# Optimization experiments

Measured on AMD Instinct MI355X. Metric: run time of the kernel, lower is better.

The kernel has to match this reference:

```python
import jax, jax.numpy as jnp
import numpy as np

# Object condensation loss config (matches init_kwargs / HGCalML defaults)
Q_MIN = 0.5
S_B = 1.0
POT_SCALE = 1.0
REP_SCALE = 1.0
BETA_SCALE = 1.0
E_WEIGHT = 1.0
HUBER_DELTA = 2.0
E_DEN_OFFSET = 1.0
K_MAX = 192          # object-id slots per event; id 0 = noise
EPS = 1e-6

B, N = 4, 50000


def setup_inputs() -> dict:
    key = jax.random.key(0)
    k1, k2, k3, k4, k5 = jax.random.split(key, 5)
    return {
        "beta": jax.random.uniform(k1, (B, N, 1), dtype=jnp.float32),
        "ccoords": jax.random.normal(k2, (B, N, 2), dtype=jnp.float32),
        "pred_energy": jax.random.uniform(k3, (B, N, 1), dtype=jnp.float32),
        "true_energy": jax.random.uniform(k4, (B, N, 1), dtype=jnp.float32),
        "truth_idx": jax.random.randint(k5, (B, N), 0, K_MAX, dtype=jnp.int32),
    }


def _per_event(beta, ccoords, pred_e, true_e, tidx):
    # beta: [N,1], ccoords: [N,2], tidx: [N] int (0 = noise)
    beta = jnp.clip(beta[:, 0], 1e-4, 1.0 - 1e-4)            # [N]
    q = jnp.arctanh(beta) ** 2 + Q_MIN                        # charge  [N]

    ids = jnp.arange(K_MAX)
    M = (tidx[:, None] == ids[None, :]) & (ids[None, :] > 0)  # [N,K] membership
    Mf = M.astype(q.dtype)
    obj_valid = jnp.any(M, axis=0)                            # [K]
    vf = obj_valid.astype(q.dtype)

    # condensation point alpha_k = argmax_q over members of object k
    qM = jnp.where(M, q[:, None], -1.0)                       # [N,K]
    idx_alpha = jnp.argmax(qM, axis=0)                        # [K]
    x_alpha = ccoords[idx_alpha]                              # [K,2]
    q_alpha = q[idx_alpha]                                    # [K]
    beta_alpha = beta[idx_alpha]                              # [K]

    # pairwise hit<->condensation-point distances
    d2 = jnp.sum((ccoords[:, None, :] - x_alpha[None, :, :]) ** 2, axis=-1)  # [N,K]

    # attractive potential (members), repulsive hinge (non-members of valid objects)
    att = jnp.sum(d2 * q_alpha[None, :] * Mf, axis=-1)                       # [N]
    dist = jnp.sqrt(d2 + EPS)
    rep = jnp.sum(jnp.maximum(0.0, 1.0 - dist) * q_alpha[None, :]
                  * (1.0 - Mf) * vf[None, :], axis=-1)                       # [N]
    L_V = jnp.mean(q * (POT_SCALE * att + REP_SCALE * rep))

    n_obj = jnp.sum(vf) + EPS
    L_beta = BETA_SCALE * jnp.sum((1.0 - beta_alpha) * vf) / n_obj

    noise = (tidx == 0).astype(q.dtype)
    L_noise = S_B * jnp.sum(beta * noise) / (jnp.sum(noise) + EPS)

    # energy payload loss: relative error, Huber, beta-weighted per object
    ediff = (pred_e[:, 0] - true_e[:, 0]) / (true_e[:, 0] + E_DEN_OFFSET)
    ad = jnp.abs(ediff)
    eh = jnp.where(ad <= HUBER_DELTA, 0.5 * ad ** 2,
                   HUBER_DELTA * (ad - 0.5 * HUBER_DELTA))                   # [N]
    pw = Mf * beta[:, None]                                                  # [N,K]
    per_obj_e = jnp.sum(pw * eh[:, None], axis=0) / (jnp.sum(pw, axis=0) + EPS)
    L_E = E_WEIGHT * jnp.sum(per_obj_e * vf) / n_obj

    return L_V + L_beta + L_noise + L_E


def reference(beta, ccoords, pred_energy, true_energy, truth_idx):
    per_ev = jax.vmap(_per_event)(beta, ccoords, pred_energy, true_energy, truth_idx)
    return jnp.mean(per_ev)
```

## Files before the change

kernel.cpp:

```cpp
#include <hip/hip_runtime.h>
#include <math.h>

#define KM 192
#define EPSF 1e-6f
#define QMIN 0.5f

__device__ __forceinline__ float clipb(float b) {
    return fminf(fmaxf(b, 1e-4f), 1.0f - 1e-4f);
}

__global__ void k_zero(unsigned int* p, int n) {
    int i = blockIdx.x * blockDim.x + threadIdx.x;
    if (i < n) p[i] = 0u;
}

__global__ void k_argmax(const float* __restrict__ beta, const int* __restrict__ tidx,
                         unsigned long long* __restrict__ packs, int N) {
    const int e = blockIdx.y;
    __shared__ unsigned long long smax[KM];
    for (int k = threadIdx.x; k < KM; k += blockDim.x) smax[k] = 0ull;
    __syncthreads();

    const float* b = beta + (size_t)e * N;
    const int*   t = tidx + (size_t)e * N;
    const int stride = gridDim.x * blockDim.x;
    for (int i = blockIdx.x * blockDim.x + threadIdx.x; i < N; i += stride) {
        int k = t[i];
        if (k > 0) {
            float bc = clipb(b[i]);
            float a  = atanhf(bc);
            float q  = a * a + QMIN;
            unsigned long long pack =
                ((unsigned long long)__float_as_uint(q) << 32) |
                (unsigned long long)(unsigned)(N - 1 - i);
            atomicMax(&smax[k], pack);
        }
    }
    __syncthreads();
    for (int k = threadIdx.x; k < KM; k += blockDim.x)
        if (smax[k]) atomicMax(&packs[e * KM + k], smax[k]);
}

__global__ void k_gather(const float* __restrict__ beta, const float* __restrict__ cc,
                         const unsigned long long* __restrict__ packs,
                         float* __restrict__ xa0, float* __restrict__ xa1,
                         float* __restrict__ qv,  float* __restrict__ vf,
                         float* __restrict__ scal, int N) {
    const int e = blockIdx.x;
    const int k = threadIdx.x;
    float lb = 0.f, nv = 0.f;
    if (k < KM) {
        unsigned long long p = packs[e * KM + k];
        float x0 = 0.f, x1 = 0.f, q = 0.f, v = 0.f;
        if (p) {
            int idx = N - 1 - (int)(unsigned)(p & 0xffffffffull);
            q  = __uint_as_float((unsigned)(p >> 32));
            x0 = cc[((size_t)e * N + idx) * 2 + 0];
            x1 = cc[((size_t)e * N + idx) * 2 + 1];
            float bc = clipb(beta[(size_t)e * N + idx]);
            lb = 1.0f - bc;
            v = 1.f; nv = 1.f;
        }
        xa0[e * KM + k] = x0;
        xa1[e * KM + k] = x1;
        qv [e * KM + k] = q * v;
        vf [e * KM + k] = v;
    }
    __shared__ float r1[256], r2[256];
    r1[threadIdx.x] = lb; r2[threadIdx.x] = nv;
    __syncthreads();
    for (int s = 128; s > 0; s >>= 1) {
        if (threadIdx.x < s) { r1[threadIdx.x] += r1[threadIdx.x + s];
                               r2[threadIdx.x] += r2[threadIdx.x + s]; }
        __syncthreads();
    }
    if (threadIdx.x == 0) { scal[e * 8 + 1] = r1[0];
                            scal[e * 8 + 2] = r2[0]; }
}

__global__ void k_main(const float* __restrict__ beta, const float* __restrict__ cc,
                       const float* __restrict__ pe,   const float* __restrict__ te,
                       const int* __restrict__ tidx,
                       const float* __restrict__ xa0, const float* __restrict__ xa1,
                       const float* __restrict__ qv,
                       float* __restrict__ enum_, float* __restrict__ eden,
                       float* __restrict__ scal, int N) {
    const int e = blockIdx.y;
    __shared__ float s0[KM], s1[KM], sq[KM];
    __shared__ float sn[KM], sd[KM];
    for (int k = threadIdx.x; k < KM; k += blockDim.x) {
        s0[k] = xa0[e * KM + k];
        s1[k] = xa1[e * KM + k];
        sq[k] = qv [e * KM + k];
        sn[k] = 0.f; sd[k] = 0.f;
    }
    __syncthreads();

    float lv = 0.f, bn = 0.f, cn = 0.f;
    const size_t base = (size_t)e * N;
    const int stride = gridDim.x * blockDim.x;
    for (int i = blockIdx.x * blockDim.x + threadIdx.x; i < N; i += stride) {
        float bc = clipb(beta[base + i]);
        float a  = atanhf(bc);
        float q  = a * a + QMIN;
        float cx = cc[(base + i) * 2 + 0];
        float cy = cc[(base + i) * 2 + 1];
        int   t  = tidx[base + i];

        float rep = 0.f;
        #pragma unroll 8
        for (int k = 0; k < KM; ++k) {
            float dx = cx - s0[k], dy = cy - s1[k];
            float d2 = dx * dx + dy * dy;
            float w  = 1.0f - sqrtf(d2 + EPSF);
            rep += fmaxf(w, 0.f) * sq[k];
        }

        float att = 0.f;
        if (t > 0) {
            float dx = cx - s0[t], dy = cy - s1[t];
            float d2 = dx * dx + dy * dy;
            att = d2 * sq[t];
            rep -= fmaxf(1.0f - sqrtf(d2 + EPSF), 0.f) * sq[t];

            float edv = (pe[base + i] - te[base + i]) / (te[base + i] + 1.0f);
            float ad  = fabsf(edv);
            float eh  = (ad <= 2.0f) ? 0.5f * ad * ad : 2.0f * (ad - 1.0f);
            atomicAdd(&sn[t], bc * eh);
            atomicAdd(&sd[t], bc);
        } else {
            bn += bc; cn += 1.f;
        }
        lv += q * (att + rep);
    }
    __syncthreads();

    for (int k = threadIdx.x; k < KM; k += blockDim.x) {
        if (sn[k] != 0.f) atomicAdd(&enum_[e * KM + k], sn[k]);
        if (sd[k] != 0.f) atomicAdd(&eden[e * KM + k], sd[k]);
    }

    __shared__ float ra[256], rb[256], rc[256];
    ra[threadIdx.x] = lv; rb[threadIdx.x] = bn; rc[threadIdx.x] = cn;
    __syncthreads();
    for (int s = 128; s > 0; s >>= 1) {
        if (threadIdx.x < s) { ra[threadIdx.x] += ra[threadIdx.x + s];
                               rb[threadIdx.x] += rb[threadIdx.x + s];
                               rc[threadIdx.x] += rc[threadIdx.x + s]; }
        __syncthreads();
    }
    if (threadIdx.x == 0) {
        atomicAdd(&scal[e * 8 + 0], ra[0]);
        atomicAdd(&scal[e * 8 + 3], rb[0]);
        atomicAdd(&scal[e * 8 + 4], rc[0]);
    }
}

__global__ void k_fin(const float* __restrict__ enum_, const float* __restrict__ eden,
                      const float* __restrict__ vf,    const float* __restrict__ scal,
                      float* __restrict__ out, int B, int N) {
    __shared__ float r[256];
    float tot = 0.f;
    for (int e = 0; e < B; ++e) {
        float le = 0.f;
        for (int k = threadIdx.x; k < KM; k += blockDim.x)
            le += vf[e * KM + k] * enum_[e * KM + k] / (eden[e * KM + k] + EPSF);
        r[threadIdx.x] = le;
        __syncthreads();
        for (int s = 128; s > 0; s >>= 1) {
            if (threadIdx.x < s) r[threadIdx.x] += r[threadIdx.x + s];
            __syncthreads();
        }
        if (threadIdx.x == 0) {
            float nobj = scal[e * 8 + 2] + EPSF;
            float LV = scal[e * 8 + 0] / (float)N;
            float LB = scal[e * 8 + 1] / nobj;
            float LN = scal[e * 8 + 3] / (scal[e * 8 + 4] + EPSF);
            float LE = r[0] / nobj;
            tot += LV + LB + LN + LE;
        }
        __syncthreads();
    }
    if (threadIdx.x == 0) out[0] = tot / (float)B;
}

extern "C" void kernel_launch(void* const* d_in, const int* in_sizes, int n_in,
                              void* d_out, int out_size, void* d_ws, size_t ws_size,
                              hipStream_t stream) {
    const int B = 4;
    const int N = in_sizes[0] / B;

    const float* beta = (const float*)d_in[0];
    const float* cc   = (const float*)d_in[1];
    const float* pe   = (const float*)d_in[2];
    const float* te   = (const float*)d_in[3];
    const int*   tidx = (const int*)  d_in[4];
    float* out = (float*)d_out;

    char* ws = (char*)d_ws;
    unsigned long long* packs = (unsigned long long*)ws;
    float* xa0  = (float*)(ws + (size_t)B * KM * 8);
    float* xa1  = xa0  + B * KM;
    float* qv   = xa1  + B * KM;
    float* vf   = qv   + B * KM;
    float* enm  = vf   + B * KM;
    float* eden = enm  + B * KM;
    float* scal = eden + B * KM;
    const int totalWords = (B * KM * 8) / 4 + B * KM * 6 + B * 8;

    k_zero<<<dim3((totalWords + 255) / 256), dim3(256), 0, stream>>>((unsigned int*)ws, totalWords);
    k_argmax<<<dim3(64, B), dim3(256), 0, stream>>>(beta, tidx, packs, N);
    k_gather<<<dim3(B), dim3(256), 0, stream>>>(beta, cc, packs, xa0, xa1, qv, vf, scal, N);
    k_main<<<dim3(128, B), dim3(256), 0, stream>>>(beta, cc, pe, te, tidx, xa0, xa1, qv, enm, eden, scal, N);
    k_fin<<<dim3(1), dim3(256), 0, stream>>>(enm, eden, vf, scal, out, B, N);
}
```

Before: 118.7 us.

## Fuse gather and finalize into main kernel, one hit per thread

Removes the gather and finalize kernels: the main kernel now decodes condensation points straight from the argmax packs into a float4 shared table, and the last block (found with an atomic counter) computes the final loss. Both argmax and main switch to one hit per thread with many more blocks; main uses 128-thread blocks with wave shuffle reductions and four partial accumulators in the 192-object loop. Zeroing becomes a hipMemsetAsync. This cuts launch count and raises occupancy, at the cost of more per-block shared-memory setup and more global atomics.

```diff
diff --git a/kernel.cpp b/kernel.cpp
--- a/kernel.cpp
+++ b/kernel.cpp
@@ -4,14 +4,10 @@
 #define KM 192
 #define EPSF 1e-6f
 #define QMIN 0.5f
+#define BLK_MAIN 128
 
 __device__ __forceinline__ float clipb(float b) {
     return fminf(fmaxf(b, 1e-4f), 1.0f - 1e-4f);
-}
-
-__global__ void k_zero(unsigned int* p, int n) {
-    int i = blockIdx.x * blockDim.x + threadIdx.x;
-    if (i < n) p[i] = 0u;
 }
 
 __global__ void k_argmax(const float* __restrict__ beta, const int* __restrict__ tidx,
@@ -20,14 +16,11 @@
     __shared__ unsigned long long smax[KM];
     for (int k = threadIdx.x; k < KM; k += blockDim.x) smax[k] = 0ull;
     __syncthreads();
-
-    const float* b = beta + (size_t)e * N;
-    const int*   t = tidx + (size_t)e * N;
-    const int stride = gridDim.x * blockDim.x;
-    for (int i = blockIdx.x * blockDim.x + threadIdx.x; i < N; i += stride) {
-        int k = t[i];
+    const int i = blockIdx.x * blockDim.x + threadIdx.x;
+    if (i < N) {
+        int k = tidx[(size_t)e * N + i];
         if (k > 0) {
-            float bc = clipb(b[i]);
+            float bc = clipb(beta[(size_t)e * N + i]);
             float a  = atanhf(bc);
             float q  = a * a + QMIN;
             unsigned long long pack =
@@ -41,65 +34,38 @@
         if (smax[k]) atomicMax(&packs[e * KM + k], smax[k]);
 }
 
-__global__ void k_gather(const float* __restrict__ beta, const float* __restrict__ cc,
-                         const unsigned long long* __restrict__ packs,
-                         float* __restrict__ xa0, float* __restrict__ xa1,
-                         float* __restrict__ qv,  float* __restrict__ vf,
-                         float* __restrict__ scal, int N) {
-    const int e = blockIdx.x;
-    const int k = threadIdx.x;
-    float lb = 0.f, nv = 0.f;
-    if (k < KM) {
+__global__ void __launch_bounds__(BLK_MAIN)
+k_main(const float* __restrict__ beta, const float* __restrict__ cc,
+       const float* __restrict__ pe,   const float* __restrict__ te,
+       const int* __restrict__ tidx,
+       const unsigned long long* __restrict__ packs,
+       float* __restrict__ enm, float* __restrict__ eden,
+       float* __restrict__ scal, unsigned int* __restrict__ cnt,
+       float* __restrict__ out, int N, int B) {
+    const int e = blockIdx.y;
+    __shared__ float4 sa[KM];
+    __shared__ float  sn[KM], sd[KM];
+    __shared__ float  swred[6];
+    __shared__ int    lastFlag;
+
+    for (int k = threadIdx.x; k < KM; k += BLK_MAIN) {
         unsigned long long p = packs[e * KM + k];
-        float x0 = 0.f, x1 = 0.f, q = 0.f, v = 0.f;
+        float x0 = 0.f, x1 = 0.f, qv = 0.f;
         if (p) {
             int idx = N - 1 - (int)(unsigned)(p & 0xffffffffull);
-            q  = __uint_as_float((unsigned)(p >> 32));
             x0 = cc[((size_t)e * N + idx) * 2 + 0];
             x1 = cc[((size_t)e * N + idx) * 2 + 1];
-            float bc = clipb(beta[(size_t)e * N + idx]);
-            lb = 1.0f - bc;
-            v = 1.f; nv = 1.f;
-        }
-        xa0[e * KM + k] = x0;
-        xa1[e * KM + k] = x1;
-        qv [e * KM + k] = q * v;
-        vf [e * KM + k] = v;
-    }
-    __shared__ float r1[256], r2[256];
-    r1[threadIdx.x] = lb; r2[threadIdx.x] = nv;
-    __syncthreads();
-    for (int s = 128; s > 0; s >>= 1) {
-        if (threadIdx.x < s) { r1[threadIdx.x] += r1[threadIdx.x + s];
-                               r2[threadIdx.x] += r2[threadIdx.x + s]; }
-        __syncthreads();
-    }
-    if (threadIdx.x == 0) { scal[e * 8 + 1] = r1[0];
-                            scal[e * 8 + 2] = r2[0]; }
-}
-
-__global__ void k_main(const float* __restrict__ beta, const float* __restrict__ cc,
-                       const float* __restrict__ pe,   const float* __restrict__ te,
-                       const int* __restrict__ tidx,
-                       const float* __restrict__ xa0, const float* __restrict__ xa1,
-                       const float* __restrict__ qv,
-                       float* __restrict__ enum_, float* __restrict__ eden,
-                       float* __restrict__ scal, int N) {
-    const int e = blockIdx.y;
-    __shared__ float s0[KM], s1[KM], sq[KM];
-    __shared__ float sn[KM], sd[KM];
-    for (int k = threadIdx.x; k < KM; k += blockDim.x) {
-        s0[k] = xa0[e * KM + k];
-        s1[k] = xa1[e * KM + k];
-        sq[k] = qv [e * KM + k];
+            qv = __uint_as_float((unsigned)(p >> 32));
+        }
+        sa[k] = make_float4(x0, x1, qv, 0.f);
         sn[k] = 0.f; sd[k] = 0.f;
     }
     __syncthreads();
 
+    const size_t base = (size_t)e * N;
+    const int i = blockIdx.x * BLK_MAIN + threadIdx.x;
     float lv = 0.f, bn = 0.f, cn = 0.f;
-    const size_t base = (size_t)e * N;
-    const int stride = gridDim.x * blockDim.x;
-    for (int i = blockIdx.x * blockDim.x + threadIdx.x; i < N; i += stride) {
+    if (i < N) {
         float bc = clipb(beta[base + i]);
         float a  = atanhf(bc);
         float q  = a * a + QMIN;
@@ -107,76 +73,105 @@
         float cy = cc[(base + i) * 2 + 1];
         int   t  = tidx[base + i];
 
-        float rep = 0.f;
-        #pragma unroll 8
+        float racc[4] = {0.f, 0.f, 0.f, 0.f};
+        #pragma unroll 16
         for (int k = 0; k < KM; ++k) {
-            float dx = cx - s0[k], dy = cy - s1[k];
-            float d2 = dx * dx + dy * dy;
-            float w  = 1.0f - sqrtf(d2 + EPSF);
-            rep += fmaxf(w, 0.f) * sq[k];
-        }
+            float4 av = sa[k];
+            float dx = cx - av.x, dy = cy - av.y;
+            float d2 = fmaf(dx, dx, fmaf(dy, dy, EPSF));
+            racc[k & 3] += fmaxf(1.f - sqrtf(d2), 0.f) * av.z;
+        }
+        float rep = (racc[0] + racc[1]) + (racc[2] + racc[3]);
 
         float att = 0.f;
         if (t > 0) {
-            float dx = cx - s0[t], dy = cy - s1[t];
-            float d2 = dx * dx + dy * dy;
-            att = d2 * sq[t];
-            rep -= fmaxf(1.0f - sqrtf(d2 + EPSF), 0.f) * sq[t];
-
-            float edv = (pe[base + i] - te[base + i]) / (te[base + i] + 1.0f);
+            float4 ao = sa[t];
+            float dx = cx - ao.x, dy = cy - ao.y;
+            float d2e = fmaf(dx, dx, fmaf(dy, dy, EPSF));
+            rep -= fmaxf(1.f - sqrtf(d2e), 0.f) * ao.z;
+            att  = fmaf(dx, dx, dy * dy) * ao.z;
+
+            float tev = te[base + i];
+            float edv = (pe[base + i] - tev) / (tev + 1.f);
             float ad  = fabsf(edv);
-            float eh  = (ad <= 2.0f) ? 0.5f * ad * ad : 2.0f * (ad - 1.0f);
+            float eh  = (ad <= 2.f) ? 0.5f * ad * ad : 2.f * (ad - 1.f);
             atomicAdd(&sn[t], bc * eh);
             atomicAdd(&sd[t], bc);
         } else {
-            bn += bc; cn += 1.f;
-        }
-        lv += q * (att + rep);
-    }
-    __syncthreads();
-
-    for (int k = threadIdx.x; k < KM; k += blockDim.x) {
-        if (sn[k] != 0.f) atomicAdd(&enum_[e * KM + k], sn[k]);
-        if (sd[k] != 0.f) atomicAdd(&eden[e * KM + k], sd[k]);
-    }
-
-    __shared__ float ra[256], rb[256], rc[256];
-    ra[threadIdx.x] = lv; rb[threadIdx.x] = bn; rc[threadIdx.x] = cn;
-    __syncthreads();
-    for (int s = 128; s > 0; s >>= 1) {
-        if (threadIdx.x < s) { ra[threadIdx.x] += ra[threadIdx.x + s];
-                               rb[threadIdx.x] += rb[threadIdx.x + s];
-                               rc[threadIdx.x] += rc[threadIdx.x + s]; }
+            bn = bc; cn = 1.f;
+        }
+        lv = q * (att + rep);
+    }
+    __syncthreads();
+
+    for (int k = threadIdx.x; k < KM; k += BLK_MAIN) {
+        float vd = sd[k];
+        if (vd != 0.f) {
+            atomicAdd(&enm [e * KM + k], sn[k]);
+            atomicAdd(&eden[e * KM + k], vd);
+        }
+    }
+
+    for (int off = 32; off > 0; off >>= 1) {
+        lv += __shfl_down(lv, off);
+        bn += __shfl_down(bn, off);
+        cn += __shfl_down(cn, off);
+    }
+    const int wid = threadIdx.x >> 6;
+    if ((threadIdx.x & 63) == 0) {
+        swred[wid] = lv; swred[2 + wid] = bn; swred[4 + wid] = cn;
+    }
+    __syncthreads();
+    if (threadIdx.x == 0) {
+        atomicAdd(&scal[e * 8 + 0], swred[0] + swred[1]);
+        atomicAdd(&scal[e * 8 + 3], swred[2] + swred[3]);
+        atomicAdd(&scal[e * 8 + 4], swred[4] + swred[5]);
+    }
+
+    if (threadIdx.x == 0) {
+        __threadfence();
+        unsigned int total = gridDim.x * gridDim.y;
+        unsigned int old = atomicAdd(cnt, 1u);
+        lastFlag = (old == total - 1u);
+    }
+    __syncthreads();
+    if (!lastFlag) return;
+
+    __threadfence();
+    volatile float* venm  = enm;
+    volatile float* veden = eden;
+    volatile float* vscal = scal;
+
+    float tot = 0.f;
+    for (int ev = 0; ev < B; ++ev) {
+        float lb = 0.f, nv = 0.f, le = 0.f;
+        for (int k = threadIdx.x; k < KM; k += BLK_MAIN) {
+            unsigned long long p = packs[ev * KM + k];
+            if (p) {
+                int idx = N - 1 - (int)(unsigned)(p & 0xffffffffull);
+                lb += 1.f - clipb(beta[(size_t)ev * N + idx]);
+                nv += 1.f;
+                le += venm[ev * KM + k] / (veden[ev * KM + k] + EPSF);
+            }
+        }
+        for (int off = 32; off > 0; off >>= 1) {
+            lb += __shfl_down(lb, off);
+            nv += __shfl_down(nv, off);
+            le += __shfl_down(le, off);
+        }
         __syncthreads();
-    }
-    if (threadIdx.x == 0) {
-        atomicAdd(&scal[e * 8 + 0], ra[0]);
-        atomicAdd(&scal[e * 8 + 3], rb[0]);
-        atomicAdd(&scal[e * 8 + 4], rc[0]);
-    }
-}
-
-__global__ void k_fin(const float* __restrict__ enum_, const float* __restrict__ eden,
-                      const float* __restrict__ vf,    const float* __restrict__ scal,
-                      float* __restrict__ out, int B, int N) {
-    __shared__ float r[256];
-    float tot = 0.f;
-    for (int e = 0; e < B; ++e) {
-        float le = 0.f;
-        for (int k = threadIdx.x; k < KM; k += blockDim.x)
-            le += vf[e * KM + k] * enum_[e * KM + k] / (eden[e * KM + k] + EPSF);
-        r[threadIdx.x] = le;
+        if ((threadIdx.x & 63) == 0) {
+            sn[threadIdx.x >> 6] = lb; sn[2 + (threadIdx.x >> 6)] = nv;
+            sn[4 + (threadIdx.x >> 6)] = le;
+        }
         __syncthreads();
-        for (int s = 128; s > 0; s >>= 1) {
-            if (threadIdx.x < s) r[threadIdx.x] += r[threadIdx.x + s];
-            __syncthreads();
-        }
         if (threadIdx.x == 0) {
-            float nobj = scal[e * 8 + 2] + EPSF;
-            float LV = scal[e * 8 + 0] / (float)N;
-            float LB = scal[e * 8 + 1] / nobj;
-            float LN = scal[e * 8 + 3] / (scal[e * 8 + 4] + EPSF);
-            float LE = r[0] / nobj;
+            float lbs = sn[0] + sn[1], nvs = sn[2] + sn[3], les = sn[4] + sn[5];
+            float nobj = nvs + EPSF;
+            float LV = vscal[ev * 8 + 0] / (float)N;
+            float LB = lbs / nobj;
+            float LN = vscal[ev * 8 + 3] / (vscal[ev * 8 + 4] + EPSF);
+            float LE = les / nobj;
             tot += LV + LB + LN + LE;
         }
         __syncthreads();
@@ -199,18 +194,15 @@
 
     char* ws = (char*)d_ws;
     unsigned long long* packs = (unsigned long long*)ws;
-    float* xa0  = (float*)(ws + (size_t)B * KM * 8);
-    float* xa1  = xa0  + B * KM;
-    float* qv   = xa1  + B * KM;
-    float* vf   = qv   + B * KM;
-    float* enm  = vf   + B * KM;
-    float* eden = enm  + B * KM;
+    float* enm  = (float*)(ws + (size_t)B * KM * 8);
+    float* eden = enm + B * KM;
     float* scal = eden + B * KM;
-    const int totalWords = (B * KM * 8) / 4 + B * KM * 6 + B * 8;
-
-    k_zero<<<dim3((totalWords + 255) / 256), dim3(256), 0, stream>>>((unsigned int*)ws, totalWords);
-    k_argmax<<<dim3(64, B), dim3(256), 0, stream>>>(beta, tidx, packs, N);
-    k_gather<<<dim3(B), dim3(256), 0, stream>>>(beta, cc, packs, xa0, xa1, qv, vf, scal, N);
-    k_main<<<dim3(128, B), dim3(256), 0, stream>>>(beta, cc, pe, te, tidx, xa0, xa1, qv, enm, eden, scal, N);
-    k_fin<<<dim3(1), dim3(256), 0, stream>>>(enm, eden, vf, scal, out, B, N);
-}
+    unsigned int* cnt = (unsigned int*)(scal + B * 8);
+    const size_t zeroBytes = (size_t)B * KM * 8 + (size_t)B * KM * 4 * 2
+                           + (size_t)B * 8 * 4 + 64;
+
+    (void)hipMemsetAsync(d_ws, 0, zeroBytes, stream);
+    k_argmax<<<dim3((N + 255) / 256, B), dim3(256), 0, stream>>>(beta, tidx, packs, N);
+    k_main<<<dim3((N + BLK_MAIN - 1) / BLK_MAIN, B), dim3(BLK_MAIN), 0, stream>>>(
+        beta, cc, pe, te, tidx, packs, enm, eden, scal, cnt, out, N, B);
+}
```

New measurement: 148.8 us. +25.3%, slower.
